# Kernel tuning notes

Hardware: AMD Instinct MI355X
Metric: run time of the kernel (lower is better)

Reference implementation:

```python
import jax, jax.numpy as jnp
import numpy as np

STATE_DIM = 256
HID_DIM = 1024
BATCH = 65536
IN_DIM = 2 * STATE_DIM + 1


def setup_inputs() -> dict:
    key = jax.random.key(0)
    ks = jax.random.split(key, 11)
    x0 = jax.random.normal(ks[0], (BATCH, STATE_DIM), dtype=jnp.float32)
    x1 = jax.random.normal(ks[1], (BATCH, STATE_DIM), dtype=jnp.float32)
    t = jax.random.uniform(ks[2], (BATCH, 1), dtype=jnp.float32)

    def linear_init(k, fan_in, fan_out):
        kw, kb = jax.random.split(k)
        bound = 1.0 / np.sqrt(fan_in)
        W = jax.random.uniform(kw, (fan_in, fan_out), minval=-bound, maxval=bound, dtype=jnp.float32)
        b = jax.random.uniform(kb, (fan_out,), minval=-bound, maxval=bound, dtype=jnp.float32)
        return W, b

    W1, b1 = linear_init(ks[3], IN_DIM, HID_DIM)
    W2, b2 = linear_init(ks[4], HID_DIM, HID_DIM)
    W3, b3 = linear_init(ks[5], HID_DIM, HID_DIM)
    W4, b4 = linear_init(ks[6], HID_DIM, STATE_DIM)
    return {"x0": x0, "x1": x1, "t": t,
            "W1": W1, "b1": b1, "W2": W2, "b2": b2,
            "W3": W3, "b3": b3, "W4": W4, "b4": b4}


def _mlp(z, W1, b1, W2, b2, W3, b3, W4, b4):
    h = jax.nn.relu(z @ W1 + b1)
    h = jax.nn.relu(h @ W2 + b2)
    h = jax.nn.relu(h @ W3 + b3)
    return h @ W4 + b4  # [B, state_dim]


def reference(x0, x1, t, W1, b1, W2, b2, W3, b3, W4, b4):
    z = jnp.concatenate((x0, x1, t), axis=1)  # [B, 2*D+1]
    # d(fnn)/dt == last column of the per-sample Jacobian; compute it with one
    # forward-mode JVP using the one-hot tangent on the t slot (fuses with fwd).
    tz = jnp.zeros_like(z).at[:, -1].set(1.0)
    fnn, dt_fnn = jax.jvp(lambda zz: _mlp(zz, W1, b1, W2, b2, W3, b3, W4, b4), (z,), (tz,))
    xt = (1.0 - t) * x0 + t * x1 + t * (1.0 - t) * fnn
    dt_xt = x1 - x0 + (1.0 - t) * fnn - t * fnn + t * (1.0 - t) * dt_fnn
    return (xt, dt_xt)
```

## Files before the change

### kernel.cpp

```cpp
#include <hip/hip_runtime.h>
#include <stdint.h>
#include <stddef.h>


typedef unsigned short u16;
typedef __attribute__((ext_vector_type(8))) short short8;
typedef __attribute__((ext_vector_type(4))) float f32x4;

#define BATCH 65536
#define SDIM 256
#define HDIM 1024

__device__ __forceinline__ u16 f2bf(float f) {
  unsigned int u = __float_as_uint(f);
  u += 0x7FFFu + ((u >> 16) & 1u);
  return (u16)(u >> 16);
}

__device__ __forceinline__ void gload_lds16(const void* g, void* l) {
  __builtin_amdgcn_global_load_lds(
      (const __attribute__((address_space(1))) unsigned int*)g,
      (__attribute__((address_space(3))) unsigned int*)l, 16, 0, 0);
}

struct EpiArgs {
  const float* bias;
  const float* r1;
  const float* t;
  const float* x0;
  const float* x1;
  u16*   out_h;
  float* out_xt;
  float* out_dt;
};

template <int EPI>
__global__ __launch_bounds__(512, 2)
void fgemm8(const u16* __restrict__ A, const u16* __restrict__ Bt,
            int N, int K, EpiArgs e)
{
  __shared__ __align__(16) u16 lds[65536];

  const int tid  = threadIdx.x;
  const int wave = tid >> 6;
  const int lane = tid & 63;
  const int hi   = lane >> 4;
  const int ln   = lane & 15;
  const int srow = lane >> 3;
  const int ssc  = lane & 7;
  const int lcs  = (ssc ^ srow) * 8;

  const int nbx = gridDim.x;
  int bx = blockIdx.x, by = blockIdx.y;
  if ((gridDim.y & 7) == 0) {
    const int id = by * nbx + bx;
    const int g  = id & 7;
    const int s  = id >> 3;
    bx = s % nbx;
    by = (s / nbx) * 8 + g;
  }
  const int bn = bx * 256;
  const int bm = by * 256;

  const int wm = (wave >> 2) * 128;
  const int wn = (wave & 3) * 64;

  f32x4 acc[8][4] = {};

  const u16* gA = A  + (size_t)bm * K + lcs;
  const u16* gB = Bt + (size_t)bn * K + lcs;
  const int NT = K >> 6;

  auto STAGE = [&](int t) {
    const int kk0 = t << 6;
    const int lb  = (t & 1) << 15;
#pragma unroll
    for (int c = 0; c < 4; ++c) {
      const int ch  = (wave << 2) + c;
      const int row = (ch << 3) + srow;
      gload_lds16(gA + (size_t)row * K + kk0, &lds[lb + ch * 512]);
      gload_lds16(gB + (size_t)row * K + kk0, &lds[lb + 16384 + ch * 512]);
    }
  };

  STAGE(0);
  STAGE(1);

  for (int t = 0; t < NT; ++t) {
    const int lb = (t & 1) << 15;
    if (t >= 1 && t + 1 < NT) STAGE(t + 1);
    if (t + 1 < NT) asm volatile("s_waitcnt vmcnt(8)" ::: "memory");
    else            asm volatile("s_waitcnt vmcnt(0)" ::: "memory");
    __builtin_amdgcn_s_barrier();

#pragma unroll
    for (int p = 0; p < 4; ++p) {
      const int mbase = (p >> 1) * 4;
      const int nbase = (p & 1) * 2;
      short8 ah[4][2], bb[2][2];
#pragma unroll
      for (int i = 0; i < 4; ++i) {
        const int row = wm + (mbase + i) * 16 + ln;
#pragma unroll
        for (int kh = 0; kh < 2; ++kh) {
          const int scs = (((kh << 2) + hi) ^ (ln & 7)) * 8;
          ah[i][kh] = *(const short8*)&lds[lb + row * 64 + scs];
        }
      }
#pragma unroll
      for (int j = 0; j < 2; ++j) {
        const int row = wn + (nbase + j) * 16 + ln;
#pragma unroll
        for (int kh = 0; kh < 2; ++kh) {
          const int scs = (((kh << 2) + hi) ^ (ln & 7)) * 8;
          bb[j][kh] = *(const short8*)&lds[lb + 16384 + row * 64 + scs];
        }
      }
      __builtin_amdgcn_s_barrier();
      asm volatile("s_waitcnt lgkmcnt(0)");
      __builtin_amdgcn_s_setprio(1);
#pragma unroll
      for (int i = 0; i < 4; ++i)
#pragma unroll
        for (int j = 0; j < 2; ++j) {
          acc[mbase + i][nbase + j] = __builtin_amdgcn_mfma_f32_16x16x32_bf16(
              ah[i][0], bb[j][0], acc[mbase + i][nbase + j], 0, 0, 0);
          acc[mbase + i][nbase + j] = __builtin_amdgcn_mfma_f32_16x16x32_bf16(
              ah[i][1], bb[j][1], acc[mbase + i][nbase + j], 0, 0, 0);
        }
      __builtin_amdgcn_s_setprio(0);
      __builtin_amdgcn_s_barrier();
    }
  }

  if constexpr (EPI == 0) {
#pragma unroll
    for (int mi = 0; mi < 8; ++mi) {
#pragma unroll
      for (int ni = 0; ni < 4; ++ni) {
        const int n = bn + wn + ni * 16 + ln;
        const float bnv = e.bias[n];
        const float r1n = e.r1[n];
#pragma unroll
        for (int r = 0; r < 4; ++r) {
          const int m = bm + wm + mi * 16 + hi * 4 + r;
          const float pre = acc[mi][ni][r] + bnv + e.t[m] * r1n;
          const size_t sH = (size_t)(m >> 4) * 32 + (m & 15);
          e.out_h[sH * (size_t)N + n]        = f2bf(fmaxf(pre, 0.f));
          e.out_h[(sH + 16) * (size_t)N + n] = (pre > 0.f) ? f2bf(r1n) : (u16)0;
        }
      }
    }
  } else if constexpr (EPI == 1) {
#pragma unroll
    for (int j = 0; j < 4; ++j) {
#pragma unroll
      for (int ni = 0; ni < 4; ++ni) {
        const int n = bn + wn + ni * 16 + ln;
        const float bnv = e.bias[n];
#pragma unroll
        for (int r = 0; r < 4; ++r) {
          const size_t sH = (size_t)(bm + wm + j * 32 + hi * 4 + r);
          const float pre = acc[2 * j][ni][r] + bnv;
          const float vu  = acc[2 * j + 1][ni][r];
          e.out_h[sH * (size_t)N + n]        = f2bf(fmaxf(pre, 0.f));
          e.out_h[(sH + 16) * (size_t)N + n] = (pre > 0.f) ? f2bf(vu) : (u16)0;
        }
      }
    }
  } else {
#pragma unroll
    for (int j = 0; j < 4; ++j) {
#pragma unroll
      for (int ni = 0; ni < 4; ++ni) {
        const int n = bn + wn + ni * 16 + ln;
        const float bnv = e.bias[n];
#pragma unroll
        for (int r = 0; r < 4; ++r) {
          const int sH = bm + wm + j * 32 + hi * 4 + r;
          const int m  = ((sH >> 5) << 4) + (hi * 4 + r);
          const float fnn = acc[2 * j][ni][r] + bnv;
          const float dtf = acc[2 * j + 1][ni][r];
          const float tt  = e.t[m];
          const size_t ix = (size_t)m * 256 + n;
          const float a = e.x0[ix], b = e.x1[ix];
          const float w = tt * (1.f - tt);
          e.out_xt[ix] = (1.f - tt) * a + tt * b + w * fnn;
          e.out_dt[ix] = b - a + (1.f - 2.f * tt) * fnn + w * dtf;
        }
      }
    }
  }
}

__global__ void prep_z(const float* __restrict__ x0, const float* __restrict__ x1,
                       u16* __restrict__ A0)
{
  const int idx = blockIdx.x * blockDim.x + threadIdx.x;
  const int m = idx >> 7;
  const int c = idx & 127;
  const float* src = (c < 64) ? (x0 + (size_t)m * 256 + c * 4)
                              : (x1 + (size_t)m * 256 + (c - 64) * 4);
  const float4 v = *(const float4*)src;
  uint2 pk;
  pk.x = (unsigned)f2bf(v.x) | ((unsigned)f2bf(v.y) << 16);
  pk.y = (unsigned)f2bf(v.z) | ((unsigned)f2bf(v.w) << 16);
  *(uint2*)&A0[(size_t)m * 512 + c * 4] = pk;
}

__global__ void transpose_cast(const float* __restrict__ W, u16* __restrict__ Wt,
                               int K, int N)
{
  __shared__ float tile[32][33];
  const int tx = threadIdx.x & 31;
  const int ty = threadIdx.x >> 5;
  const int k0 = blockIdx.x * 32;
  const int n0 = blockIdx.y * 32;
#pragma unroll
  for (int i = 0; i < 32; i += 8)
    tile[ty + i][tx] = W[(size_t)(k0 + ty + i) * N + n0 + tx];
  __syncthreads();
#pragma unroll
  for (int i = 0; i < 32; i += 8)
    Wt[(size_t)(n0 + ty + i) * K + k0 + tx] = f2bf(tile[tx][ty + i]);
}

extern "C" void kernel_launch(void* const* d_in, const int* in_sizes, int n_in,
                              void* d_out, int out_size, void* d_ws, size_t ws_size,
                              hipStream_t stream)
{
  const float* x0 = (const float*)d_in[0];
  const float* x1 = (const float*)d_in[1];
  const float* t  = (const float*)d_in[2];
  const float* W1 = (const float*)d_in[3];
  const float* b1 = (const float*)d_in[4];
  const float* W2 = (const float*)d_in[5];
  const float* b2 = (const float*)d_in[6];
  const float* W3 = (const float*)d_in[7];
  const float* b3 = (const float*)d_in[8];
  const float* W4 = (const float*)d_in[9];
  const float* b4 = (const float*)d_in[10];

  char* ws = (char*)d_ws;
  const size_t WB1 = (size_t)512 * HDIM * 2;
  const size_t WB2 = (size_t)HDIM * HDIM * 2;
  const size_t WB4 = (size_t)HDIM * SDIM * 2;
  u16* Wt1 = (u16*)(ws);
  u16* Wt2 = (u16*)(ws + WB1);
  u16* Wt3 = (u16*)(ws + WB1 + WB2);
  u16* Wt4 = (u16*)(ws + WB1 + 2 * WB2);
  const size_t wmark = WB1 + 2 * WB2 + WB4;
  char* act = ws + wmark;

  int nc = 1;
  while (nc < 64 && wmark + (size_t)(BATCH / nc) * 8192 > ws_size) nc <<= 1;
  const int CB = BATCH / nc;

  u16* Sa = (u16*)(act);
  u16* Sb = (u16*)(act + (size_t)CB * 4096);
  u16* Zc = Sb;

  transpose_cast<<<dim3(16, 32), 256, 0, stream>>>(W1, Wt1, 512, HDIM);
  transpose_cast<<<dim3(32, 32), 256, 0, stream>>>(W2, Wt2, HDIM, HDIM);
  transpose_cast<<<dim3(32, 32), 256, 0, stream>>>(W3, Wt3, HDIM, HDIM);
  transpose_cast<<<dim3(32, 8),  256, 0, stream>>>(W4, Wt4, HDIM, SDIM);

  const float* r1 = W1 + (size_t)512 * HDIM;
  float* out_xt = (float*)d_out;
  float* out_dt = (float*)d_out + (size_t)BATCH * SDIM;

  for (int c = 0; c < nc; ++c) {
    const size_t mb = (size_t)c * CB;

    prep_z<<<(CB * 128) / 256, 256, 0, stream>>>(x0 + mb * SDIM, x1 + mb * SDIM, Zc);

    { EpiArgs e{}; e.bias = b1; e.r1 = r1; e.t = t + mb; e.out_h = Sa;
      fgemm8<0><<<dim3(HDIM / 256, CB / 256), 512, 0, stream>>>(Zc, Wt1, HDIM, 512, e); }

    { EpiArgs e{}; e.bias = b2; e.out_h = Sb;
      fgemm8<1><<<dim3(HDIM / 256, CB / 128), 512, 0, stream>>>(Sa, Wt2, HDIM, HDIM, e); }

    { EpiArgs e{}; e.bias = b3; e.out_h = Sa;
      fgemm8<1><<<dim3(HDIM / 256, CB / 128), 512, 0, stream>>>(Sb, Wt3, HDIM, HDIM, e); }

    { EpiArgs e{}; e.bias = b4; e.t = t + mb;
      e.x0 = x0 + mb * SDIM; e.x1 = x1 + mb * SDIM;
      e.out_xt = out_xt + mb * SDIM; e.out_dt = out_dt + mb * SDIM;
      fgemm8<2><<<dim3(SDIM / 256, CB / 128), 512, 0, stream>>>(Sa, Wt4, SDIM, HDIM, e); }
  }
}
```

Measured before the change: 1.238 ms.

## Restructure GEMM K-loop: split by k-half, fewer barriers, prefetch after compute

Reorganizes the inner GEMM tile loop. It now iterates over two k-halves, loading all 8 A and 4 B fragments per half, instead of four quadrant passes that each carried two barriers. The next-next stage prefetch into the just-consumed LDS buffer is issued after a single end-of-iteration barrier, replacing the prefetch at loop top. The aim is to cut barrier count and let LDS reads overlap MFMA without per-phase lgkmcnt(0) waits. In exchange it raises register pressure from holding 12 fragments live, and it changes when the global-to-LDS loads are in flight relative to the vmcnt waits.

```diff
diff --git a/kernel.cpp b/kernel.cpp
--- a/kernel.cpp
+++ b/kernel.cpp
@@ -87,50 +87,36 @@
   STAGE(1);
 
   for (int t = 0; t < NT; ++t) {
-    const int lb = (t & 1) << 15;
-    if (t >= 1 && t + 1 < NT) STAGE(t + 1);
     if (t + 1 < NT) asm volatile("s_waitcnt vmcnt(8)" ::: "memory");
     else            asm volatile("s_waitcnt vmcnt(0)" ::: "memory");
     __builtin_amdgcn_s_barrier();
-
-#pragma unroll
-    for (int p = 0; p < 4; ++p) {
-      const int mbase = (p >> 1) * 4;
-      const int nbase = (p & 1) * 2;
-      short8 ah[4][2], bb[2][2];
-#pragma unroll
-      for (int i = 0; i < 4; ++i) {
-        const int row = wm + (mbase + i) * 16 + ln;
-#pragma unroll
-        for (int kh = 0; kh < 2; ++kh) {
-          const int scs = (((kh << 2) + hi) ^ (ln & 7)) * 8;
-          ah[i][kh] = *(const short8*)&lds[lb + row * 64 + scs];
-        }
-      }
-#pragma unroll
-      for (int j = 0; j < 2; ++j) {
-        const int row = wn + (nbase + j) * 16 + ln;
-#pragma unroll
-        for (int kh = 0; kh < 2; ++kh) {
-          const int scs = (((kh << 2) + hi) ^ (ln & 7)) * 8;
-          bb[j][kh] = *(const short8*)&lds[lb + 16384 + row * 64 + scs];
-        }
-      }
-      __builtin_amdgcn_s_barrier();
-      asm volatile("s_waitcnt lgkmcnt(0)");
+    __builtin_amdgcn_sched_barrier(0);
+
+    const int lb = (t & 1) << 15;
+#pragma unroll
+    for (int kh = 0; kh < 2; ++kh) {
+      const int scs = (((kh << 2) + hi) ^ (ln & 7)) * 8;
+      short8 a8[8], b8[4];
+#pragma unroll
+      for (int i = 0; i < 8; ++i)
+        a8[i] = *(const short8*)&lds[lb + (wm + i * 16 + ln) * 64 + scs];
+#pragma unroll
+      for (int j = 0; j < 4; ++j)
+        b8[j] = *(const short8*)&lds[lb + 16384 + (wn + j * 16 + ln) * 64 + scs];
       __builtin_amdgcn_s_setprio(1);
 #pragma unroll
-      for (int i = 0; i < 4; ++i)
-#pragma unroll
-        for (int j = 0; j < 2; ++j) {
-          acc[mbase + i][nbase + j] = __builtin_amdgcn_mfma_f32_16x16x32_bf16(
-              ah[i][0], bb[j][0], acc[mbase + i][nbase + j], 0, 0, 0);
-          acc[mbase + i][nbase + j] = __builtin_amdgcn_mfma_f32_16x16x32_bf16(
-              ah[i][1], bb[j][1], acc[mbase + i][nbase + j], 0, 0, 0);
-        }
+      for (int i = 0; i < 8; ++i)
+#pragma unroll
+        for (int j = 0; j < 4; ++j)
+          acc[i][j] = __builtin_amdgcn_mfma_f32_16x16x32_bf16(
+              a8[i], b8[j], acc[i][j], 0, 0, 0);
       __builtin_amdgcn_s_setprio(0);
-      __builtin_amdgcn_s_barrier();
-    }
+    }
+
+    __builtin_amdgcn_sched_barrier(0);
+    __builtin_amdgcn_s_barrier();
+    __builtin_amdgcn_sched_barrier(0);
+    if (t + 2 < NT) STAGE(t + 2);
   }
 
   if constexpr (EPI == 0) {
```

New measurement: 1.096 ms. 1.13x faster.
